# Optimization experiments

Measured on AMD Instinct MI355X. Metric: run time of the kernel, lower is better.

The kernel has to match this reference:

```python
import jax, jax.numpy as jnp
import numpy as np

A = 3                      # anchors per location
HS = [256, 128, 64, 32]    # square feature-map sizes (FPN levels)
B = 4                      # batch (num images)
SIZES = [A * h * h for h in HS]
T = sum(SIZES)             # 261120 anchors per image
PRE_N, POST_N = 512, 512
NMS_TH, SCORE_TH, MIN_SIZE = 0.7, 0.0, 1e-3
LOG_MAX = 4.135166556742356   # log(1000/16), standard delta clamp
MAXV = 8                      # max vertices of quad-quad intersection
LVL_OFF = 8192.0              # per-level coordinate offset for batched NMS


def box_corners(b):
    # b: [..., 5] (cx, cy, w, h, angle) -> [..., 4, 2] CCW corners
    cx, cy, w, h, a = (b[..., i] for i in range(5))
    c, s = jnp.cos(a), jnp.sin(a)
    dx = 0.5 * jnp.stack([w, -w, -w, w], -1)
    dy = 0.5 * jnp.stack([h, h, -h, -h], -1)
    x = cx[..., None] + dx * c[..., None] - dy * s[..., None]
    y = cy[..., None] + dx * s[..., None] + dy * c[..., None]
    return jnp.stack([x, y], -1)


def _clip(poly, cnt, p1, p2):
    # Sutherland-Hodgman clip of poly (padded [MAXV,2], cnt valid) by half-plane left of p1->p2
    e = p2 - p1
    d = e[0] * (poly[:, 1] - p1[1]) - e[1] * (poly[:, 0] - p1[0])
    def body(carry, i):
        out, oc = carry
        nxt = jnp.where(i + 1 < cnt, i + 1, 0)
        cur_in, nxt_in = d[i] >= 0, d[nxt] >= 0
        valid = i < cnt
        keep = valid & cur_in
        out = out.at[oc].set(jnp.where(keep, poly[i], out[oc]))
        oc = oc + keep.astype(jnp.int32)
        crs = valid & (cur_in != nxt_in)
        den = d[i] - d[nxt]
        t = d[i] / jnp.where(den == 0, 1.0, den)
        ip = poly[i] + t * (poly[nxt] - poly[i])
        out = out.at[oc].set(jnp.where(crs, ip, out[oc]))
        oc = oc + crs.astype(jnp.int32)
        return (out, oc), None
    (out, oc), _ = jax.lax.scan(body, (jnp.zeros((MAXV, 2), poly.dtype), jnp.int32(0)), jnp.arange(MAXV))
    return out, oc


def _inter_area(ca, cb):
    # intersection area of two convex quads given CCW corners [4,2]
    poly = jnp.zeros((MAXV, 2), ca.dtype).at[:4].set(ca)
    cnt = jnp.int32(4)
    for k in range(4):
        poly, cnt = _clip(poly, cnt, cb[k], cb[(k + 1) % 4])
    i = jnp.arange(MAXV)
    nxt = jnp.where(i + 1 < cnt, i + 1, 0)
    cr = poly[i, 0] * poly[nxt, 1] - poly[nxt, 0] * poly[i, 1]
    area = 0.5 * jnp.abs(jnp.sum(jnp.where(i < cnt, cr, 0.0)))
    return jnp.where(cnt >= 3, area, 0.0)


def decode(deltas, anchors):
    # XYWHA decode with 6-dim deltas (dx,dy,dw,dh,dsin,dcos), weights all 1.0
    ax, ay, aw, ah, aa = (anchors[..., i] for i in range(5))
    dx, dy, dw, dh, ds, dc = (deltas[..., i] for i in range(6))
    dw = jnp.minimum(dw, LOG_MAX)
    dh = jnp.minimum(dh, LOG_MAX)
    return jnp.stack([ax + dx * aw, ay + dy * ah, aw * jnp.exp(dw),
                      ah * jnp.exp(dh), aa + jnp.arctan2(ds, dc)], -1)


def nms_image(boxes, scores, levels):
    # boxes [N,5], scores [N] (post-sigmoid), levels [N] int32 -> fixed-size padded outputs
    N = scores.shape[0]
    valid = (boxes[:, 2] >= MIN_SIZE) & (boxes[:, 3] >= MIN_SIZE) & (scores >= SCORE_TH)
    s = jnp.where(valid, scores, -jnp.inf)
    order = jnp.argsort(-s)
    bx, sc, vd = boxes[order], s[order], valid[order]
    off = levels[order].astype(bx.dtype) * LVL_OFF
    nb = bx.at[:, :2].add(off[:, None])          # level offset => cross-level IoU == 0
    nbg = jax.lax.stop_gradient(nb)
    corners = box_corners(nbg)                    # [N,4,2]
    areas = nbg[:, 2] * nbg[:, 3]
    CH = 128
    def chunk_fn(args):
        cc, ca = args
        def row(ci, ai):
            inter = jax.vmap(lambda cj: _inter_area(ci, cj))(corners)
            return inter / (ai + areas - inter + 1e-7)
        return jax.vmap(row)(cc, ca)
    iou = jax.lax.map(chunk_fn, (corners.reshape(N // CH, CH, 4, 2),
                                 areas.reshape(N // CH, CH))).reshape(N, N)
    idx = jnp.arange(N)
    def body(i, sup):
        keep_i = ~sup[i]
        return sup | (keep_i & (iou[i] > NMS_TH) & (idx > i))
    sup = jax.lax.fori_loop(0, N, body, ~vd)      # invalid boxes start suppressed
    kept = ~sup
    _, top_i = jax.lax.top_k(jnp.where(kept, sc, -jnp.inf), POST_N)
    ok = kept[top_i]
    return jnp.where(ok[:, None], bx[top_i], 0.0), jnp.where(ok, sc[top_i], 0.0)


def rpn_forward(objs, dlts, anchors):
    obj_f, dlt_f = [], []
    for o, d, h in zip(objs, dlts, HS):
        # permute_and_flatten: [B,A,H,W] -> [B,H*W*A]; [B,A*6,H,W] -> [B,H*W*A,6]
        obj_f.append(o.transpose(0, 2, 3, 1).reshape(B, -1))
        dlt_f.append(d.reshape(B, A, 6, h, h).transpose(0, 3, 4, 1, 2).reshape(B, -1, 6))
    objectness = jnp.concatenate(obj_f, 1)        # [B, T]
    deltas = jnp.concatenate(dlt_f, 1)            # [B, T, 6]
    proposals = decode(deltas, anchors)           # [B, T, 5]
    parts, offset = [], 0
    for sz in SIZES:                               # per-level top-k
        k = min(PRE_N, sz)
        _, ti = jax.lax.top_k(objectness[:, offset:offset + sz], k)
        parts.append(ti + offset)
        offset += sz
    top_idx = jnp.concatenate(parts, 1)           # [B, 4*PRE_N]
    levels = jnp.concatenate([jnp.full((sz,), i, jnp.int32) for i, sz in enumerate(SIZES)])
    obj_top = jnp.take_along_axis(objectness, top_idx, 1)
    prop_top = jnp.take_along_axis(proposals, top_idx[..., None], 1)
    lvl_top = levels[top_idx]
    scores = jax.nn.sigmoid(obj_top)
    return jax.vmap(nms_image)(prop_top, scores, lvl_top)


def setup_inputs() -> dict:
    key = jax.random.key(0)
    ks = jax.random.split(key, 9)
    inp = {}
    for i, h in enumerate(HS):
        inp[f"obj{i}"] = jax.random.normal(ks[i], (B, A, h, h), jnp.float32)
        inp[f"dlt{i}"] = 0.25 * jax.random.normal(ks[4 + i], (B, A * 6, h, h), jnp.float32)
    u = jax.random.uniform(ks[8], (B, T, 5), jnp.float32)
    inp["anchors"] = jnp.stack([u[..., 0] * 1024.0, u[..., 1] * 1024.0,
                                8.0 + 120.0 * u[..., 2], 8.0 + 120.0 * u[..., 3],
                                jnp.pi * (u[..., 4] - 0.5)], -1)
    return inp


def reference(obj0, obj1, obj2, obj3, dlt0, dlt1, dlt2, dlt3, anchors):
    # returns (boxes [B, POST_N, 5], scores [B, POST_N]) padded with zeros
    return rpn_forward([obj0, obj1, obj2, obj3], [dlt0, dlt1, dlt2, dlt3], anchors)
```

## Files before the change

kernel.cpp:

```cpp
#include <hip/hip_runtime.h>

typedef unsigned int u32;
typedef unsigned long long u64;
typedef unsigned char u8;

#define NB 4
#define T_ANCH 261120
#define NCAND 2048
#define KSEL 512
#define POSTN 512
#define LOG_MAXF 4.135166556742356f
#define NMS_TH 0.7f
#define LVL_OFF_F 8192.0f
#define BINS 4096
#define EQCAP 8192
#define K5_BLOCKS 2048
#define K1_BLOCKS 256

__device__ __forceinline__ u32 mono32(float f){
  u32 u = __float_as_uint(f);
  return (u & 0x80000000u) ? ~u : (u | 0x80000000u);
}
__device__ __forceinline__ int lvl_hw(int lvl){ return 65536 >> (2*lvl); }
__device__ __forceinline__ int lvl_off(int lvl){
  return (lvl>0?196608:0) + (lvl>1?49152:0) + (lvl>2?12288:0);
}
__device__ __forceinline__ void k1_map(int bx, int& b, int& lvl, int& ch){
  b = bx >> 6;
  int c = bx & 63;
  if (c < 48){ lvl = 0; ch = c; }
  else if (c < 60){ lvl = 1; ch = c - 48; }
  else if (c < 63){ lvl = 2; ch = c - 60; }
  else { lvl = 3; ch = 0; }
}

__global__ __launch_bounds__(1024) void k1_hist_thresh(
    const float* __restrict__ o0, const float* __restrict__ o1,
    const float* __restrict__ o2, const float* __restrict__ o3,
    u32* __restrict__ hist16, u32* __restrict__ done16,
    u32* __restrict__ gb0, u32* __restrict__ gcA)
{
  int b, lvl, ch;
  k1_map(blockIdx.x, b, lvl, ch);
  int bid16 = b*4 + lvl;
  int nch = (lvl==0?48 : lvl==1?12 : lvl==2?3 : 1);
  const float* ob = (lvl==0)?o0 : (lvl==1)?o1 : (lvl==2)?o2 : o3;
  int hw = lvl_hw(lvl);
  int size = 3*hw;
  int n4 = size >> 2;
  int i4 = ch*1024 + threadIdx.x;
  __shared__ u32 hist[BINS];
  __shared__ u32 coarse[64];
  __shared__ int s_last;
  for (int i = threadIdx.x; i < BINS; i += 1024) hist[i] = 0;
  __syncthreads();
  if (i4 < n4){
    float4 v = ((const float4*)(ob + (size_t)b*size))[i4];
    atomicAdd(&hist[mono32(v.x) >> 20], 1u);
    atomicAdd(&hist[mono32(v.y) >> 20], 1u);
    atomicAdd(&hist[mono32(v.z) >> 20], 1u);
    atomicAdd(&hist[mono32(v.w) >> 20], 1u);
  }
  __syncthreads();
  u32* gh = hist16 + (size_t)bid16*BINS;
  for (int i = threadIdx.x; i < BINS; i += 1024){
    u32 c = hist[i];
    if (c) atomicAdd(&gh[i], c);
  }
  __syncthreads();
  if (threadIdx.x == 0){
    __threadfence();
    u32 d = atomicAdd(&done16[bid16], 1u);
    s_last = (d == (u32)(nch - 1)) ? 1 : 0;
  }
  __syncthreads();
  if (!s_last) return;

  __threadfence();
  for (int i = threadIdx.x; i < BINS; i += 1024)
    hist[i] = __hip_atomic_load(&gh[i], __ATOMIC_RELAXED, __HIP_MEMORY_SCOPE_AGENT);
  __syncthreads();
  int t = threadIdx.x;
  if (t < 64){
    u32 s = 0;
    for (int z = 0; z < 64; ++z) s += hist[t*64 + z];
    coarse[t] = s;
  }
  __syncthreads();
  if (t == 0){
    u32 acc = 0;
    int cb = 63;
    while (acc + coarse[cb] < (u32)KSEL){ acc += coarse[cb]; --cb; }
    int z = cb*64 + 63;
    while (acc + hist[z] < (u32)KSEL){ acc += hist[z]; --z; }
    gb0[bid16] = (u32)z;
    gcA[bid16] = acc;
  }
}

__global__ __launch_bounds__(1024) void k2_classify(
    const float* __restrict__ o0, const float* __restrict__ o1,
    const float* __restrict__ o2, const float* __restrict__ o3,
    const u32* __restrict__ gb0,
    u32* __restrict__ emitcnt, u32* __restrict__ tiecnt,
    int* __restrict__ cand_j, u64* __restrict__ gtie)
{
  int b, lvl, ch;
  k1_map(blockIdx.x, b, lvl, ch);
  int bid16 = b*4 + lvl;
  const float* ob = (lvl==0)?o0 : (lvl==1)?o1 : (lvl==2)?o2 : o3;
  int hw = lvl_hw(lvl);
  int size = 3*hw;
  int n4 = size >> 2;
  int i4 = ch*1024 + threadIdx.x;

  __shared__ u32 dbuf[KSEL];
  __shared__ u64 tbuf[4096];
  __shared__ u32 dn, tn, dbase, tbase;
  if (threadIdx.x == 0){ dn = 0; tn = 0; }
  __syncthreads();

  u32 b0v = gb0[bid16];
  if (i4 < n4){
    float4 v = ((const float4*)(ob + (size_t)b*size))[i4];
    int L = i4 << 2;
    int a = L / hw;
    int pix = L - a*hw;
    int j0 = pix*3 + a;
    float vv[4] = {v.x, v.y, v.z, v.w};
    #pragma unroll
    for (int q = 0; q < 4; ++q){
      u32 m = mono32(vv[q]);
      u32 bin = m >> 20;
      int j = j0 + 3*q;
      if (bin > b0v){
        u32 s = atomicAdd(&dn, 1u);
        if (s < (u32)KSEL) dbuf[s] = (u32)j;
      } else if (bin == b0v){
        u32 s = atomicAdd(&tn, 1u);
        if (s < 4096u) tbuf[s] = ((u64)m << 32) | (u32)(~(u32)j);
      }
    }
  }
  __syncthreads();
  if (threadIdx.x == 0){
    dbase = dn ? atomicAdd(&emitcnt[bid16], dn) : 0u;
    tbase = tn ? atomicAdd(&tiecnt[bid16], tn) : 0u;
  }
  __syncthreads();
  for (u32 x = threadIdx.x; x < dn; x += 1024){
    u32 s = dbase + x;
    if (s < (u32)KSEL) cand_j[bid16*KSEL + s] = (int)dbuf[x];
  }
  for (u32 x = threadIdx.x; x < tn; x += 1024){
    u32 s = tbase + x;
    if (s < (u32)EQCAP) gtie[(size_t)bid16*EQCAP + s] = tbuf[x];
  }
}

__global__ __launch_bounds__(512) void k3_tie_decode(
    const u64* __restrict__ gtie, const u32* __restrict__ tiecnt,
    const u32* __restrict__ gcA, const int* __restrict__ cand_j,
    const float* __restrict__ o0, const float* __restrict__ o1,
    const float* __restrict__ o2, const float* __restrict__ o3,
    const float* __restrict__ d0, const float* __restrict__ d1,
    const float* __restrict__ d2, const float* __restrict__ d3,
    const float* __restrict__ anchors,
    float* __restrict__ cscore, u32* __restrict__ csmono,
    u64* __restrict__ ctb, float* __restrict__ cbox, u8* __restrict__ cvalid)
{
  int bid = blockIdx.x;
  int t = threadIdx.x;
  __shared__ u64 eq[EQCAP];
  __shared__ u32 wbuf[KSEL];
  __shared__ int jlist[KSEL];
  __shared__ u32 wn;
  u32 n = tiecnt[bid]; if (n > (u32)EQCAP) n = (u32)EQCAP;
  u32 cA = gcA[bid];
  u32 k = (u32)KSEL - cA;
  if (t == 0) wn = 0;
  for (int i = t; i < KSEL; i += 512) jlist[i] = 0;
  for (u32 i = t; i < n; i += 512) eq[i] = gtie[(size_t)bid*EQCAP + i];
  __syncthreads();
  for (u32 i = t; i < n; i += 512){
    u64 ki = eq[i];
    u32 r = 0;
    for (u32 m = 0; m < n; ++m) r += (eq[m] > ki) ? 1u : 0u;
    if (r < k){
      u32 s = atomicAdd(&wn, 1u);
      if (s < (u32)KSEL) wbuf[s] = (u32)(~(u32)ki);
    }
  }
  __syncthreads();
  u32 w = wn;
  for (u32 i = t; i < cA; i += 512)
    if (i < (u32)KSEL) jlist[i] = cand_j[bid*KSEL + i];
  for (u32 x = t; x < w; x += 512){
    u32 s = cA + x;
    if (s < (u32)KSEL) jlist[s] = (int)wbuf[x];
  }
  __syncthreads();

  {
    int c = bid*KSEL + t;
    int b = bid >> 2, lvl = bid & 3;
    int j = jlist[t];
    int hw = lvl_hw(lvl);
    u32 pix = (u32)j / 3u;
    u32 a = (u32)j - pix*3u;
    const float* ob = (lvl==0)?o0 : (lvl==1)?o1 : (lvl==2)?o2 : o3;
    const float* dl = (lvl==0)?d0 : (lvl==1)?d1 : (lvl==2)?d2 : d3;

    float ov = ob[(size_t)(b*3 + (int)a)*hw + pix];
    size_t dbase = ((size_t)(b*3 + (int)a)*6)*(size_t)hw + pix;
    float dx  = dl[dbase + 0*(size_t)hw];
    float dy  = dl[dbase + 1*(size_t)hw];
    float dw  = dl[dbase + 2*(size_t)hw];
    float dh  = dl[dbase + 3*(size_t)hw];
    float dsn = dl[dbase + 4*(size_t)hw];
    float dcs = dl[dbase + 5*(size_t)hw];
    int tt = lvl_off(lvl) + j;
    const float* an = anchors + ((size_t)b*T_ANCH + tt)*5;
    float ax=an[0], ay=an[1], aw=an[2], ah=an[3], aa=an[4];
    dw = fminf(dw, LOG_MAXF); dh = fminf(dh, LOG_MAXF);
    float cx = ax + dx*aw;
    float cy = ay + dy*ah;
    float ww = aw * expf(dw);
    float hh = ah * expf(dh);
    float ang = aa + atan2f(dsn, dcs);
    double sd = 1.0 / (1.0 + exp(-(double)ov));
    float sc = (float)sd;
    bool valid = (ww >= 1e-3f) && (hh >= 1e-3f) && (sc >= 0.0f);
    cscore[c] = sc;
    csmono[c] = valid ? mono32(sc) : 0u;
    ctb[c] = ((u64)lvl << 50) | ((u64)(u32)(~mono32(ov)) << 18) | (u64)(u32)j;
    cvalid[c] = valid ? 1 : 0;
    float* bb = cbox + (size_t)c*5;
    bb[0]=cx; bb[1]=cy; bb[2]=ww; bb[3]=hh; bb[4]=ang;
  }
}

__global__ __launch_bounds__(256) void k4_rank(
    const u32* __restrict__ csmono, const u64* __restrict__ ctb,
    const float* __restrict__ cscore, const float* __restrict__ cbox,
    const u8* __restrict__ cvalid,
    float* __restrict__ sscore, float* __restrict__ sbox,
    float* __restrict__ geom, float4* __restrict__ aabb4,
    u8* __restrict__ svalid, u64* __restrict__ maskz, u64* __restrict__ rowflagz,
    u32* __restrict__ lvlidx)
{
  int b   = blockIdx.x >> 6;
  int blk = blockIdx.x & 63;
  __shared__ u32 sm[NCAND];
  __shared__ u64 stb[NCAND];
  __shared__ u32 cnt[32][8];
  {
    u64* mz = maskz + (size_t)blockIdx.x * 1024;
    for (int x = threadIdx.x; x < 1024; x += 256) mz[x] = 0ull;
    if (threadIdx.x == 0 && blockIdx.x < NB*32) rowflagz[blockIdx.x] = 0ull;
  }
  for (int k = threadIdx.x; k < NCAND; k += 256){
    sm[k]  = csmono[b*NCAND + k];
    stb[k] = ctb[b*NCAND + k];
  }
  __syncthreads();
  int esub = threadIdx.x >> 3;
  int ssub = threadIdx.x & 7;
  int id = blk*32 + esub;
  u32 ms = sm[id];
  u64 mt = stb[id];
  u32 r = 0;
  #pragma unroll 8
  for (int it = 0; it < 256; ++it){
    int m = it*8 + ssub;
    u32 s2 = sm[m]; u64 t2 = stb[m];
    r += ((s2 > ms) || (s2 == ms && t2 < mt)) ? 1u : 0u;
  }
  cnt[esub][ssub] = r;
  __syncthreads();
  if (ssub == 0){
    u32 rank = 0;
    #pragma unroll
    for (int q = 0; q < 8; ++q) rank += cnt[esub][q];
    int gsrc = b*NCAND + id;
    int gdst = b*NCAND + (int)rank;
    sscore[gdst] = cscore[gsrc];
    svalid[gdst] = cvalid[gsrc];
    float b0 = cbox[(size_t)gsrc*5+0], b1 = cbox[(size_t)gsrc*5+1];
    float b2 = cbox[(size_t)gsrc*5+2], b3 = cbox[(size_t)gsrc*5+3];
    float b4 = cbox[(size_t)gsrc*5+4];
    float* sb = sbox + (size_t)gdst*5;
    sb[0]=b0; sb[1]=b1; sb[2]=b2; sb[3]=b3; sb[4]=b4;
    int lvl = (int)((mt >> 50) & 3ull);
    lvlidx[(u32)(b*4 + (id >> 9))*KSEL + (u32)(id & 511)] = (u32)rank;
    float offv = (float)lvl * LVL_OFF_F;
    float cx = b0 + offv, cy = b1 + offv, w=b2, h=b3, ang=b4;
    float cc = cosf(ang), sn = sinf(ang);
    float hx = 0.5f*w, hy = 0.5f*h;
    float x0 = cx + hx*cc - hy*sn, y0 = cy + hx*sn + hy*cc;
    float x1 = cx - hx*cc - hy*sn, y1 = cy - hx*sn + hy*cc;
    float x2 = cx - hx*cc + hy*sn, y2 = cy - hx*sn - hy*cc;
    float x3 = cx + hx*cc + hy*sn, y3 = cy + hx*sn - hy*cc;
    float minx = fminf(fminf(x0,x1),fminf(x2,x3));
    float maxx = fmaxf(fmaxf(x0,x1),fmaxf(x2,x3));
    float miny = fminf(fminf(y0,y1),fminf(y2,y3));
    float maxy = fmaxf(fmaxf(y0,y1),fmaxf(y2,y3));
    float* g = geom + (size_t)gdst*16;
    g[0]=minx; g[1]=maxx; g[2]=miny; g[3]=maxy; g[4]=w*h;
    g[5]=x0; g[6]=y0; g[7]=x1; g[8]=y1; g[9]=x2; g[10]=y2; g[11]=x3; g[12]=y3;
    aabb4[gdst] = make_float4(minx, maxx, miny, maxy);
  }
}

__device__ __forceinline__ void emit_pt(float* ox, float* oy, int oc, float x, float y){
  #pragma unroll
  for (int s = 0; s < 8; ++s) if (s == oc){ ox[s] = x; oy[s] = y; }
}

__device__ float quad_inter(const float* ca, const float* cb){
  float px[8], py[8];
  #pragma unroll
  for (int q = 0; q < 8; ++q){ px[q]=0.f; py[q]=0.f; }
  #pragma unroll
  for (int q = 0; q < 4; ++q){ px[q]=ca[2*q]; py[q]=ca[2*q+1]; }
  int cnt = 4;
  #pragma unroll
  for (int e = 0; e < 4; ++e){
    float p1x = cb[2*e],         p1y = cb[2*e+1];
    float p2x = cb[(2*e+2)&7],   p2y = cb[(2*e+3)&7];
    float ex = p2x-p1x, ey = p2y-p1y;
    float d[8];
    #pragma unroll
    for (int q = 0; q < 8; ++q) d[q] = ex*(py[q]-p1y) - ey*(px[q]-p1x);
    float ox[8], oy[8];
    #pragma unroll
    for (int q = 0; q < 8; ++q){ ox[q]=0.f; oy[q]=0.f; }
    int oc = 0;
    #pragma unroll
    for (int q = 0; q < 8; ++q){
      if (q < cnt){
        bool last = (q+1 >= cnt);
        float dn  = last ? d[0]  : d[(q+1)&7];
        bool in0 = (d[q] >= 0.0f), in1 = (dn >= 0.0f);
        if (in0){ emit_pt(ox,oy,oc,px[q],py[q]); oc++; }
        if (in0 != in1){
          float pnx = last ? px[0] : px[(q+1)&7];
          float pny = last ? py[0] : py[(q+1)&7];
          float den = d[q] - dn;
          float t = d[q] / ((den == 0.0f) ? 1.0f : den);
          emit_pt(ox,oy,oc, px[q] + t*(pnx-px[q]), py[q] + t*(pny-py[q]));
          oc++;
        }
      }
    }
    cnt = (oc > 8) ? 8 : oc;
    #pragma unroll
    for (int q = 0; q < 8; ++q){ px[q]=ox[q]; py[q]=oy[q]; }
  }
  if (cnt < 3) return 0.0f;
  float s = 0.0f;
  #pragma unroll
  for (int q = 0; q < 8; ++q){
    if (q < cnt){
      bool last = (q+1 >= cnt);
      float pnx = last ? px[0] : px[(q+1)&7];
      float pny = last ? py[0] : py[(q+1)&7];
      s += px[q]*pny - pnx*py[q];
    }
  }
  return 0.5f*fabsf(s);
}

__global__ __launch_bounds__(256) void k5_pairs(
    const u32* __restrict__ lvlidx,
    const float4* __restrict__ aabb4, const float* __restrict__ geom,
    u64* __restrict__ mask, u64* __restrict__ rowflag)
{
  __shared__ u32   s_idx[KSEL];
  __shared__ float4 s_ab[KSEL];
  __shared__ float  s_ar[KSEL];
  __shared__ u32   lbuf[1024];
  __shared__ u32 lcnt;
  const int t = threadIdx.x;
  if (t == 0) lcnt = 0;
  int img = blockIdx.x >> 9;
  int r9  = blockIdx.x & 511;
  int lvl = r9 >> 7;
  int kk  = r9 & 127;
  int lane = t & 63;
  const int base = (img*4 + lvl)*KSEL;
  for (int q = t; q < KSEL; q += 256){
    u32 rk = lvlidx[base + q];
    s_idx[q] = rk;
    s_ab[q]  = aabb4[img*NCAND + rk];
    s_ar[q]  = geom[((size_t)(img*NCAND + rk))*16 + 4];
  }
  __syncthreads();
  int rows[4] = {2*kk, 2*kk + 1, 510 - 2*kk, 511 - 2*kk};
  #pragma unroll
  for (int r = 0; r < 4; ++r){
    int p = rows[r];
    float4 gi = s_ab[p];
    float  ai = s_ar[p];
    for (int q = p + 1 + t; q < KSEL; q += 256){
      float4 gj = s_ab[q];
      float w = fminf(gi.y, gj.y) - fmaxf(gi.x, gj.x);
      float h = fminf(gi.w, gj.w) - fmaxf(gi.z, gj.z);
      bool pass = (w > 0.0f) && (h > 0.0f);
      if (pass){
        float iA = w*h;
        float S  = ai + s_ar[q];
        pass = ((1.0f + NMS_TH)*iA >= NMS_TH*S*(1.0f - 1e-5f));
      }
      u64 bm = __ballot(pass);
      if (bm){
        int leader = __ffsll((long long)bm) - 1;
        u32 bs = 0;
        if (lane == leader) bs = atomicAdd(&lcnt, (u32)__popcll(bm));
        bs = (u32)__shfl((int)bs, leader);
        if (pass){
          u32 off = (u32)__popcll(bm & ((1ull << lane) - 1ull));
          lbuf[bs + off] = (u32)((p << 9) | q);
        }
      }
    }
  }
  __syncthreads();
  u32 n = lcnt;
  for (u32 x = t; x < n; x += 256){
    u32 pr = lbuf[x];
    int p = (int)(pr >> 9), q = (int)(pr & 511);
    u32 ri = s_idx[p], rj = s_idx[q];
    u32 i = ri < rj ? ri : rj;
    u32 j = ri < rj ? rj : ri;
    const float* gi = geom + ((size_t)(img*NCAND + (int)i))*16;
    const float* gj = geom + ((size_t)(img*NCAND + (int)j))*16;
    float inter = quad_inter(gi+5, gj+5);
    float iou = inter / (gi[4] + gj[4] - inter + 1e-7f);
    if (iou > NMS_TH){
      atomicOr(&mask[((size_t)(img*NCAND + (int)i))*32 + (j >> 6)], 1ull << (j & 63));
      atomicOr(&rowflag[(size_t)img*32 + (i >> 6)], 1ull << (i & 63));
    }
  }
}

__global__ __launch_bounds__(1024) void k6_nms_out(
    const u64* __restrict__ mask, const u64* __restrict__ rowflag,
    const u8* __restrict__ svalid,
    const float* __restrict__ sbox, const float* __restrict__ sscore,
    float* __restrict__ out)
{
  int b = blockIdx.x;
  __shared__ u32 fid[NCAND];
  __shared__ u32 wcnt[32], wpref[32];
  __shared__ u64 s_kept[32];
  __shared__ u32 pref[32];
  __shared__ u32 s_F;
  int t = threadIdx.x;
  int wid = t >> 6, lane = t & 63;

  if (t < 32) wcnt[t] = (u32)__popcll(rowflag[b*32 + t]);
  __syncthreads();
  if (t == 0){
    u32 run = 0;
    for (int w = 0; w < 32; ++w){ wpref[w] = run; run += wcnt[w]; }
    s_F = run;
  }
  __syncthreads();
  if (t < 32){
    u64 fw = rowflag[b*32 + t];
    u32 o = wpref[t];
    while (fw){
      int bpos = __builtin_ctzll(fw);
      fid[o++] = (u32)(t*64 + bpos);
      fw &= fw - 1;
    }
  }
  for (int x = t; x < POSTN*5; x += 1024) out[(size_t)b*POSTN*5 + x] = 0.0f;
  for (int x = t; x < POSTN;   x += 1024) out[(size_t)NB*POSTN*5 + b*POSTN + x] = 0.0f;
  __syncthreads();

  if (wid == 0){
    u32 slo = 0, shi = 0;
    {
      int wl = lane & 31;
      u64 w = 0;
      for (int q = 0; q < 64; ++q)
        if (!svalid[b*NCAND + wl*64 + q]) w |= (1ull << q);
      slo = (u32)w; shi = (u32)(w >> 32);
    }
    u32 F = s_F;
    const u64* mb = mask + ((size_t)b*NCAND)*32;
    for (u32 f = 0; f < F; f += 8){
      u32 myfid = 0;
      if (f + (lane & 7) < F) myfid = fid[f + (lane & 7)];
      u64 v[8];
      #pragma unroll
      for (int q = 0; q < 8; ++q){
        if (f + q < F){
          u32 fq = (u32)__builtin_amdgcn_readlane((int)myfid, q);
          v[q] = mb[(size_t)fq*32 + (lane & 31)];
        } else v[q] = 0ull;
      }
      #pragma unroll
      for (int q = 0; q < 8; ++q){
        if (f + q < F){
          u32 i = (u32)__builtin_amdgcn_readlane((int)myfid, q);
          int wi = (int)(i >> 6);
          u32 wlo = (u32)__builtin_amdgcn_readlane((int)slo, wi);
          u32 whi = (u32)__builtin_amdgcn_readlane((int)shi, wi);
          u64 w = ((u64)whi << 32) | wlo;
          u32 keep = (u32)((~w >> (i & 63)) & 1ull);
          u64 vm = v[q] & (0ull - (u64)keep);
          slo |= (u32)vm; shi |= (u32)(vm >> 32);
        }
      }
    }
    if (lane < 32) s_kept[lane] = ~(((u64)shi << 32) | slo);
  }
  __syncthreads();

  if (t < 32) pref[t] = (u32)__popcll(s_kept[t]);
  __syncthreads();
  if (t == 0){
    u32 run = 0;
    for (int w = 0; w < 32; ++w){ u32 tv = pref[w]; pref[w] = run; run += tv; }
  }
  __syncthreads();
  for (int i = t; i < NCAND; i += 1024){
    u64 kw = s_kept[i >> 6];
    if ((kw >> (i & 63)) & 1ull){
      u32 rank = pref[i >> 6] + (u32)__popcll(kw & ((1ull << (i & 63)) - 1ull));
      if (rank < POSTN){
        const float* bp = sbox + ((size_t)(b*NCAND + i))*5;
        float* op = out + ((size_t)(b*POSTN + rank))*5;
        op[0]=bp[0]; op[1]=bp[1]; op[2]=bp[2]; op[3]=bp[3]; op[4]=bp[4];
        out[(size_t)NB*POSTN*5 + b*POSTN + rank] = sscore[b*NCAND + i];
      }
    }
  }
}

extern "C" void kernel_launch(void* const* d_in, const int* in_sizes, int n_in,
                              void* d_out, int out_size, void* d_ws, size_t ws_size,
                              hipStream_t stream)
{
  (void)out_size; (void)ws_size;
  const float *obj[4] = {nullptr,nullptr,nullptr,nullptr};
  const float *dlt[4] = {nullptr,nullptr,nullptr,nullptr};
  const float *anchors = nullptr;
  for (int i = 0; i < n_in; ++i){
    int s = in_sizes[i];
    const float* p = (const float*)d_in[i];
    switch (s){
      case 786432:  obj[0] = p; break;
      case 4718592: dlt[0] = p; break;
      case 196608:  obj[1] = p; break;
      case 1179648: dlt[1] = p; break;
      case 49152:   obj[2] = p; break;
      case 294912:  dlt[2] = p; break;
      case 12288:   obj[3] = p; break;
      case 73728:   dlt[3] = p; break;
      case 5222400: anchors = p; break;
      default: break;
    }
  }

  char* wsb = (char*)d_ws;
  size_t off = 0;
  auto alloc = [&](size_t bytes)->void*{
    size_t cur = (off + 255) & ~(size_t)255;
    off = cur + bytes;
    return (void*)(wsb + cur);
  };
  int*   cand_j = (int*)  alloc(16*KSEL*sizeof(int));
  float* cscore = (float*)alloc((size_t)NB*NCAND*sizeof(float));
  u32*   csmono = (u32*)  alloc((size_t)NB*NCAND*sizeof(u32));
  u64*   ctb    = (u64*)  alloc((size_t)NB*NCAND*sizeof(u64));
  float* cbox   = (float*)alloc((size_t)NB*NCAND*5*sizeof(float));
  u8*    cvalid = (u8*)   alloc((size_t)NB*NCAND);
  float* sscore = (float*)alloc((size_t)NB*NCAND*sizeof(float));
  float* sbox   = (float*)alloc((size_t)NB*NCAND*5*sizeof(float));
  u8*    svalid = (u8*)   alloc((size_t)NB*NCAND);
  float* geom   = (float*)alloc((size_t)NB*NCAND*16*sizeof(float));
  float4* aabb4 = (float4*)alloc((size_t)NB*NCAND*sizeof(float4));
  u64*   gtie   = (u64*)  alloc((size_t)16*EQCAP*sizeof(u64));
  u64*   maskp  = (u64*)  alloc((size_t)NB*NCAND*32*sizeof(u64));
  u64*   rowflag= (u64*)  alloc((size_t)NB*32*sizeof(u64));
  u32*   lvlidx = (u32*)  alloc((size_t)16*KSEL*sizeof(u32));
  u32*   gb0    = (u32*)  alloc(16*sizeof(u32));
  u32*   gcA    = (u32*)  alloc(16*sizeof(u32));
  u32*   hist16 = (u32*)  alloc((size_t)16*BINS*sizeof(u32));
  u32*   done16 = (u32*)  alloc(16*sizeof(u32));
  u32*   emitc  = (u32*)  alloc(16*sizeof(u32));
  u32*   tiec   = (u32*)  alloc(16*sizeof(u32));
  size_t zero_len = (size_t)((wsb + off) - (char*)hist16);

  hipMemsetAsync(hist16, 0, zero_len, stream);

  hipLaunchKernelGGL(k1_hist_thresh, dim3(K1_BLOCKS), dim3(1024), 0, stream,
                     obj[0], obj[1], obj[2], obj[3], hist16, done16, gb0, gcA);
  hipLaunchKernelGGL(k2_classify, dim3(K1_BLOCKS), dim3(1024), 0, stream,
                     obj[0], obj[1], obj[2], obj[3], gb0, emitc, tiec,
                     cand_j, gtie);
  hipLaunchKernelGGL(k3_tie_decode, dim3(16), dim3(512), 0, stream,
                     gtie, tiec, gcA, cand_j,
                     obj[0], obj[1], obj[2], obj[3],
                     dlt[0], dlt[1], dlt[2], dlt[3],
                     anchors, cscore, csmono, ctb, cbox, cvalid);
  hipLaunchKernelGGL(k4_rank, dim3(256), dim3(256), 0, stream,
                     csmono, ctb, cscore, cbox, cvalid, sscore, sbox, geom,
                     aabb4, svalid, maskp, rowflag, lvlidx);
  hipLaunchKernelGGL(k5_pairs, dim3(K5_BLOCKS), dim3(256), 0, stream,
                     lvlidx, aabb4, geom, maskp, rowflag);
  hipLaunchKernelGGL(k6_nms_out, dim3(4), dim3(1024), 0, stream,
                     maskp, rowflag, svalid, sbox, sscore, (float*)d_out);
}
```

Before: 184.6 us.

## Fuse classify and tie-decode kernels using last-block-done atomic counter

Merges the classify kernel and the tie-resolve/decode kernel into one launch. Each (image, level) group counts finished chunk blocks with an atomic counter, and the last block to finish does the tie ranking and proposal decode with a shared-memory union. This removes one kernel launch and the gap between the two launches. In exchange it adds fences and atomics, and the decode work now runs in a single tail block per group instead of a separate grid.

```diff
diff --git a/kernel.cpp b/kernel.cpp
--- a/kernel.cpp
+++ b/kernel.cpp
@@ -98,29 +98,43 @@
   }
 }
 
-__global__ __launch_bounds__(1024) void k2_classify(
+union Sh23 {
+  struct { u32 dbuf[KSEL]; u64 tbuf[4096]; } c;
+  struct { u64 eq[EQCAP]; u32 wbuf[KSEL]; int jlist[KSEL]; } p3;
+};
+
+__global__ __launch_bounds__(1024) void k23_classify_tie_decode(
     const float* __restrict__ o0, const float* __restrict__ o1,
     const float* __restrict__ o2, const float* __restrict__ o3,
-    const u32* __restrict__ gb0,
+    const float* __restrict__ d0, const float* __restrict__ d1,
+    const float* __restrict__ d2, const float* __restrict__ d3,
+    const float* __restrict__ anchors,
+    const u32* __restrict__ gb0, const u32* __restrict__ gcA,
     u32* __restrict__ emitcnt, u32* __restrict__ tiecnt,
-    int* __restrict__ cand_j, u64* __restrict__ gtie)
+    u32* __restrict__ cls_done,
+    int* __restrict__ cand_j, u64* __restrict__ gtie,
+    float* __restrict__ cscore, u32* __restrict__ csmono,
+    u64* __restrict__ ctb, float* __restrict__ cbox, u8* __restrict__ cvalid)
 {
+  __shared__ Sh23 sh;
+  __shared__ u32 s_dn, s_tn, s_dbase, s_tbase, s_wn;
+  __shared__ int s_last;
+  const int t = threadIdx.x;
   int b, lvl, ch;
   k1_map(blockIdx.x, b, lvl, ch);
-  int bid16 = b*4 + lvl;
+  const int bid16 = b*4 + lvl;
+  const int nch = (lvl==0?48 : lvl==1?12 : lvl==2?3 : 1);
   const float* ob = (lvl==0)?o0 : (lvl==1)?o1 : (lvl==2)?o2 : o3;
-  int hw = lvl_hw(lvl);
-  int size = 3*hw;
-  int n4 = size >> 2;
-  int i4 = ch*1024 + threadIdx.x;
-
-  __shared__ u32 dbuf[KSEL];
-  __shared__ u64 tbuf[4096];
-  __shared__ u32 dn, tn, dbase, tbase;
-  if (threadIdx.x == 0){ dn = 0; tn = 0; }
-  __syncthreads();
-
-  u32 b0v = gb0[bid16];
+  const int hw = lvl_hw(lvl);
+  const int size = 3*hw;
+  const int n4 = size >> 2;
+  const int i4 = ch*1024 + t;
+
+  if (t == 0){ s_dn = 0; s_tn = 0; }
+  __syncthreads();
+
+  const u32 b0v = gb0[bid16];
+  const u32 cA  = gcA[bid16];
   if (i4 < n4){
     float4 v = ((const float4*)(ob + (size_t)b*size))[i4];
     int L = i4 << 2;
@@ -134,83 +148,79 @@
       u32 bin = m >> 20;
       int j = j0 + 3*q;
       if (bin > b0v){
-        u32 s = atomicAdd(&dn, 1u);
-        if (s < (u32)KSEL) dbuf[s] = (u32)j;
+        u32 s = atomicAdd(&s_dn, 1u);
+        if (s < (u32)KSEL) sh.c.dbuf[s] = (u32)j;
       } else if (bin == b0v){
-        u32 s = atomicAdd(&tn, 1u);
-        if (s < 4096u) tbuf[s] = ((u64)m << 32) | (u32)(~(u32)j);
+        u32 s = atomicAdd(&s_tn, 1u);
+        if (s < 4096u) sh.c.tbuf[s] = ((u64)m << 32) | (u32)(~(u32)j);
       }
     }
   }
   __syncthreads();
-  if (threadIdx.x == 0){
-    dbase = dn ? atomicAdd(&emitcnt[bid16], dn) : 0u;
-    tbase = tn ? atomicAdd(&tiecnt[bid16], tn) : 0u;
-  }
-  __syncthreads();
-  for (u32 x = threadIdx.x; x < dn; x += 1024){
-    u32 s = dbase + x;
-    if (s < (u32)KSEL) cand_j[bid16*KSEL + s] = (int)dbuf[x];
-  }
-  for (u32 x = threadIdx.x; x < tn; x += 1024){
-    u32 s = tbase + x;
-    if (s < (u32)EQCAP) gtie[(size_t)bid16*EQCAP + s] = tbuf[x];
-  }
-}
-
-__global__ __launch_bounds__(512) void k3_tie_decode(
-    const u64* __restrict__ gtie, const u32* __restrict__ tiecnt,
-    const u32* __restrict__ gcA, const int* __restrict__ cand_j,
-    const float* __restrict__ o0, const float* __restrict__ o1,
-    const float* __restrict__ o2, const float* __restrict__ o3,
-    const float* __restrict__ d0, const float* __restrict__ d1,
-    const float* __restrict__ d2, const float* __restrict__ d3,
-    const float* __restrict__ anchors,
-    float* __restrict__ cscore, u32* __restrict__ csmono,
-    u64* __restrict__ ctb, float* __restrict__ cbox, u8* __restrict__ cvalid)
-{
-  int bid = blockIdx.x;
-  int t = threadIdx.x;
-  __shared__ u64 eq[EQCAP];
-  __shared__ u32 wbuf[KSEL];
-  __shared__ int jlist[KSEL];
-  __shared__ u32 wn;
-  u32 n = tiecnt[bid]; if (n > (u32)EQCAP) n = (u32)EQCAP;
-  u32 cA = gcA[bid];
+  if (t == 0){
+    s_dbase = s_dn ? atomicAdd(&emitcnt[bid16], s_dn) : 0u;
+    s_tbase = s_tn ? atomicAdd(&tiecnt[bid16], s_tn) : 0u;
+  }
+  __syncthreads();
+  for (u32 x = t; x < s_dn; x += 1024){
+    u32 s = s_dbase + x;
+    if (s < (u32)KSEL)
+      __hip_atomic_store(&cand_j[bid16*KSEL + s], (int)sh.c.dbuf[x],
+                         __ATOMIC_RELAXED, __HIP_MEMORY_SCOPE_AGENT);
+  }
+  for (u32 x = t; x < s_tn; x += 1024){
+    u32 s = s_tbase + x;
+    if (s < (u32)EQCAP)
+      __hip_atomic_store(&gtie[(size_t)bid16*EQCAP + s], sh.c.tbuf[x],
+                         __ATOMIC_RELAXED, __HIP_MEMORY_SCOPE_AGENT);
+  }
+  __syncthreads();
+  if (t == 0){
+    __threadfence();
+    u32 d = __hip_atomic_fetch_add(&cls_done[bid16], 1u,
+                                   __ATOMIC_ACQ_REL, __HIP_MEMORY_SCOPE_AGENT);
+    s_last = (d == (u32)(nch - 1)) ? 1 : 0;
+  }
+  __syncthreads();
+  if (!s_last) return;
+
+  u32 n = __hip_atomic_load(&tiecnt[bid16], __ATOMIC_RELAXED, __HIP_MEMORY_SCOPE_AGENT);
+  if (n > (u32)EQCAP) n = (u32)EQCAP;
   u32 k = (u32)KSEL - cA;
-  if (t == 0) wn = 0;
-  for (int i = t; i < KSEL; i += 512) jlist[i] = 0;
-  for (u32 i = t; i < n; i += 512) eq[i] = gtie[(size_t)bid*EQCAP + i];
-  __syncthreads();
-  for (u32 i = t; i < n; i += 512){
-    u64 ki = eq[i];
+  if (t == 0) s_wn = 0;
+  __syncthreads();
+  for (int i = t; i < KSEL; i += 1024) sh.p3.jlist[i] = 0;
+  for (u32 i = t; i < n; i += 1024)
+    sh.p3.eq[i] = __hip_atomic_load(&gtie[(size_t)bid16*EQCAP + i],
+                                    __ATOMIC_RELAXED, __HIP_MEMORY_SCOPE_AGENT);
+  __syncthreads();
+  for (u32 i = t; i < n; i += 1024){
+    u64 ki = sh.p3.eq[i];
     u32 r = 0;
-    for (u32 m = 0; m < n; ++m) r += (eq[m] > ki) ? 1u : 0u;
+    for (u32 m = 0; m < n; ++m) r += (sh.p3.eq[m] > ki) ? 1u : 0u;
     if (r < k){
-      u32 s = atomicAdd(&wn, 1u);
-      if (s < (u32)KSEL) wbuf[s] = (u32)(~(u32)ki);
-    }
-  }
-  __syncthreads();
-  u32 w = wn;
-  for (u32 i = t; i < cA; i += 512)
-    if (i < (u32)KSEL) jlist[i] = cand_j[bid*KSEL + i];
-  for (u32 x = t; x < w; x += 512){
+      u32 s = atomicAdd(&s_wn, 1u);
+      if (s < (u32)KSEL) sh.p3.wbuf[s] = (u32)(~(u32)ki);
+    }
+  }
+  __syncthreads();
+  u32 w = s_wn; if (w > (u32)KSEL) w = (u32)KSEL;
+  for (u32 i = t; i < cA; i += 1024)
+    if (i < (u32)KSEL)
+      sh.p3.jlist[i] = __hip_atomic_load(&cand_j[bid16*KSEL + i],
+                                         __ATOMIC_RELAXED, __HIP_MEMORY_SCOPE_AGENT);
+  for (u32 x = t; x < w; x += 1024){
     u32 s = cA + x;
-    if (s < (u32)KSEL) jlist[s] = (int)wbuf[x];
-  }
-  __syncthreads();
-
-  {
-    int c = bid*KSEL + t;
-    int b = bid >> 2, lvl = bid & 3;
-    int j = jlist[t];
-    int hw = lvl_hw(lvl);
+    if (s < (u32)KSEL) sh.p3.jlist[s] = (int)sh.p3.wbuf[x];
+  }
+  __syncthreads();
+
+  if (t < KSEL){
+    int c = bid16*KSEL + t;
+    int j = sh.p3.jlist[t];
     u32 pix = (u32)j / 3u;
     u32 a = (u32)j - pix*3u;
-    const float* ob = (lvl==0)?o0 : (lvl==1)?o1 : (lvl==2)?o2 : o3;
     const float* dl = (lvl==0)?d0 : (lvl==1)?d1 : (lvl==2)?d2 : d3;
-
     float ov = ob[(size_t)(b*3 + (int)a)*hw + pix];
     size_t dbase = ((size_t)(b*3 + (int)a)*6)*(size_t)hw + pix;
     float dx  = dl[dbase + 0*(size_t)hw];
@@ -592,6 +602,7 @@
   u32*   gcA    = (u32*)  alloc(16*sizeof(u32));
   u32*   hist16 = (u32*)  alloc((size_t)16*BINS*sizeof(u32));
   u32*   done16 = (u32*)  alloc(16*sizeof(u32));
+  u32*   clsdn  = (u32*)  alloc(16*sizeof(u32));
   u32*   emitc  = (u32*)  alloc(16*sizeof(u32));
   u32*   tiec   = (u32*)  alloc(16*sizeof(u32));
   size_t zero_len = (size_t)((wsb + off) - (char*)hist16);
@@ -600,14 +611,11 @@
 
   hipLaunchKernelGGL(k1_hist_thresh, dim3(K1_BLOCKS), dim3(1024), 0, stream,
                      obj[0], obj[1], obj[2], obj[3], hist16, done16, gb0, gcA);
-  hipLaunchKernelGGL(k2_classify, dim3(K1_BLOCKS), dim3(1024), 0, stream,
-                     obj[0], obj[1], obj[2], obj[3], gb0, emitc, tiec,
-                     cand_j, gtie);
-  hipLaunchKernelGGL(k3_tie_decode, dim3(16), dim3(512), 0, stream,
-                     gtie, tiec, gcA, cand_j,
+  hipLaunchKernelGGL(k23_classify_tie_decode, dim3(K1_BLOCKS), dim3(1024), 0, stream,
                      obj[0], obj[1], obj[2], obj[3],
-                     dlt[0], dlt[1], dlt[2], dlt[3],
-                     anchors, cscore, csmono, ctb, cbox, cvalid);
+                     dlt[0], dlt[1], dlt[2], dlt[3], anchors,
+                     gb0, gcA, emitc, tiec, clsdn,
+                     cand_j, gtie, cscore, csmono, ctb, cbox, cvalid);
   hipLaunchKernelGGL(k4_rank, dim3(256), dim3(256), 0, stream,
                      csmono, ctb, cscore, cbox, cvalid, sscore, sbox, geom,
                      aabb4, svalid, maskp, rowflag, lvlidx);
```

Measured after the change: 189.4 us. 1.03x slower.
